# Kernel optimization log

Hardware: AMD Instinct MI355X
Metric: run time of the kernel (lower is better)

## Reference

```python
import jax, jax.numpy as jnp
import numpy as np

B, CIN, H, W = 8, 128, 64, 64
COUT = 128
UP = 2
KH = KW = 2 * UP  # 4
K = KH * KW       # 16
HO, WO = H - KH + 1, W - KW + 1  # stride=1, padding=0 (defaults actually used)


def setup_inputs() -> dict:
    key = jax.random.key(0)
    k1, k2, k3, k4, k5 = jax.random.split(key, 5)
    inp = jax.random.normal(k1, (B, CIN, H, W), jnp.float32)
    offset = jax.random.normal(k2, (B, 2 * K, HO, WO), jnp.float32)
    mask = jax.random.uniform(k3, (B, K, HO, WO), jnp.float32)
    fan_in = CIN * KH * KW
    bound = 1.0 / np.sqrt(fan_in)  # kaiming_uniform(a=sqrt(5)) bound
    weight = jax.random.uniform(k4, (COUT, CIN, KH, KW), jnp.float32, -bound, bound)
    bias = jax.random.uniform(k5, (COUT,), jnp.float32, -bound, bound)
    return {"input": inp, "offset": offset, "mask": mask, "weight": weight, "bias": bias}


def _deform_conv(inp, offset, mask, weight, bias):
    # modulated deformable conv, groups=1, stride=1, pad=0, dilation=1
    b, cin, h, w = inp.shape
    ho, wo = offset.shape[2], offset.shape[3]
    k = mask.shape[1]
    off = offset.reshape(b, k, 2, ho, wo)
    dy, dx = off[:, :, 0], off[:, :, 1]              # [b,k,ho,wo]

    ki, kj = jnp.meshgrid(jnp.arange(KH), jnp.arange(KW), indexing="ij")
    ki = ki.reshape(k).astype(inp.dtype)
    kj = kj.reshape(k).astype(inp.dtype)

    # sampling coords: base output pixel + kernel tap + learned offset
    y = dy + ki[None, :, None, None] + jnp.arange(ho, dtype=inp.dtype)[None, None, :, None]
    x = dx + kj[None, :, None, None] + jnp.arange(wo, dtype=inp.dtype)[None, None, None, :]

    y0f = jnp.floor(y)
    x0f = jnp.floor(x)
    wy = y - y0f                                     # [b,k,ho,wo]
    wx = x - x0f
    y0 = y0f.astype(jnp.int32)
    x0 = x0f.astype(jnp.int32)

    inp_flat = inp.reshape(b, cin, h * w)

    def gather(yy, xx):
        valid = (yy >= 0) & (yy < h) & (xx >= 0) & (xx < w)
        idx = (jnp.clip(yy, 0, h - 1) * w + jnp.clip(xx, 0, w - 1)).reshape(b, -1)
        v = jnp.take_along_axis(inp_flat, idx[:, None, :], axis=2)
        v = v.reshape(b, cin, k, ho, wo)
        return v * valid[:, None].astype(inp.dtype)

    v00 = gather(y0, x0)
    v01 = gather(y0, x0 + 1)
    v10 = gather(y0 + 1, x0)
    v11 = gather(y0 + 1, x0 + 1)

    wy = wy[:, None]  # [b,1,k,ho,wo]
    wx = wx[:, None]
    sampled = (v00 * (1 - wy) * (1 - wx) + v01 * (1 - wy) * wx
               + v10 * wy * (1 - wx) + v11 * wy * wx)
    sampled = sampled * mask[:, None]                # mask modulation

    # weight is flipped in forward: weight.flip(-1, -2)
    w_flip = weight[:, :, ::-1, ::-1].reshape(weight.shape[0], cin, k)
    out = jnp.einsum("bckhw,ock->bohw", sampled, w_flip)
    return out + bias[None, :, None, None]


def reference(input, offset, mask, weight, bias):
    return _deform_conv(input, offset, mask, weight, bias)
```

## Files before the change

### kernel.cpp

```cpp
#include <hip/hip_runtime.h>
#include <hip/hip_bf16.h>

#define B_    8
#define CIN   128
#define H_    64
#define W_    64
#define COUT  128
#define K_    16
#define HO    61
#define WO    61
#define HW_   (HO * WO)

typedef short bf16x8 __attribute__((ext_vector_type(8)));
typedef short s16x4  __attribute__((ext_vector_type(4)));
typedef int   s32x4  __attribute__((ext_vector_type(4)));
typedef float f32x4  __attribute__((ext_vector_type(4)));
typedef float f32x2  __attribute__((ext_vector_type(2)));
typedef float f32x4u __attribute__((ext_vector_type(4), aligned(4)));

__global__ __launch_bounds__(256) void prep_all(const float* __restrict__ inp,
                                                const float* __restrict__ w,
                                                __hip_bfloat16* __restrict__ T,
                                                __hip_bfloat16* __restrict__ A2) {
    const int t = threadIdx.x;
    if (blockIdx.x < 512) {
        __shared__ float ld[64][129];
        const int b  = blockIdx.x >> 6;
        const int sb = (blockIdx.x & 63) << 6;
        const float* src = inp + ((size_t)b << 19);
        #pragma unroll
        for (int i = 0; i < 8; ++i) {
            int j  = i * 256 + t;
            int c  = j >> 4;
            int s4 = (j & 15) << 2;
            f32x4u v = *(const f32x4u*)(const void*)(src + ((size_t)c << 12) + sb + s4);
            #pragma unroll
            for (int q = 0; q < 4; ++q) ld[s4 + q][c] = v[q];
        }
        __syncthreads();
        __hip_bfloat16* dst = T + (((size_t)b << 12) + sb) * 128;
        #pragma unroll
        for (int i = 0; i < 8; ++i) {
            int j  = i * 256 + t;
            int s  = j >> 5;
            int c4 = (j & 31) << 2;
            s16x4 v;
            #pragma unroll
            for (int q = 0; q < 4; ++q) {
                __hip_bfloat16 hh = __float2bfloat16(ld[s][c4 + q]);
                v[q] = *reinterpret_cast<const short*>(&hh);
            }
            *(s16x4*)(void*)(dst + (size_t)s * 128 + c4) = v;
        }
    } else {
        int gid  = (blockIdx.x - 512) * 256 + t;
        int lane = gid & 63;
        int it   = (gid >> 6) & 63;
        int blk  = gid >> 12;
        int o    = blk * 16 + (lane & 15);
        int kk   = it * 32 + (lane >> 4) * 8;
        int k    = kk >> 7;
        int c0   = kk & 127;
        const float* srcw = w + (((size_t)(o << 7) + c0) << 4) + (15 - k);
        __hip_bfloat16* dst = A2 + (size_t)gid * 8;
        #pragma unroll
        for (int j = 0; j < 8; ++j)
            dst[j] = __float2bfloat16(srcw[j << 4]);
    }
}

__global__ __launch_bounds__(512, 4) void deform_gather(
        const __hip_bfloat16* __restrict__ T, const float* __restrict__ off,
        const float* __restrict__ msk, const __hip_bfloat16* __restrict__ A2,
        const float* __restrict__ bias, float* __restrict__ out) {

    __shared__ __align__(16) __hip_bfloat16 Bs[2][64 * 128];
    __shared__ float pw[4][1024];
    __shared__ int   pb[2][1024];

    const int t   = threadIdx.x;
    const int bid = blockIdx.x;
    const int b   = bid & 7;
    const int ho  = bid >> 3;

    #pragma unroll
    for (int ii = 0; ii < 2; ++ii) {
        const int idx = ii * 512 + t;
        const int px  = idx & 63;
        const int k   = idx >> 6;
        const bool pvalid = (px < WO);
        const int wo_c = pvalid ? px : (WO - 1);
        const int r    = ho * WO + wo_c;
        const int ki = k >> 2, kj = k & 3;
        const size_t offb = (size_t)b * (2 * K_ * HW_);
        float dy = off[offb + (size_t)(2 * k)     * HW_ + r];
        float dx = off[offb + (size_t)(2 * k + 1) * HW_ + r];
        float mm = msk[(size_t)b * (K_ * HW_) + (size_t)k * HW_ + r];
        if (!pvalid) mm = 0.0f;

        float y   = dy + (float)(ki + ho);
        float x   = dx + (float)(kj + wo_c);
        float y0f = floorf(y), x0f = floorf(x);
        float wy  = y - y0f,   wx  = x - x0f;
        int y0 = (int)y0f, x0 = (int)x0f;
        int y1 = y0 + 1,   x1 = x0 + 1;

        float wy0v = (1.0f - wy) * ((y0 >= 0 && y0 < H_) ? mm : 0.0f);
        float wy1v = wy          * ((y1 >= 0 && y1 < H_) ? mm : 0.0f);
        int cy0 = min(max(y0, 0), H_ - 1), cy1 = min(max(y1, 0), H_ - 1);

        float wx0v = (1.0f - wx) * ((x0 >= 0 && x0 < W_) ? 1.0f : 0.0f);
        float wx1v = wx          * ((x1 >= 0 && x1 < W_) ? 1.0f : 0.0f);
        int xb = min(max(x0, 0), W_ - 2);
        int tsh = x0 - xb;
        float a0 = (tsh == 0) ? wx0v : ((tsh == -1) ? wx1v : 0.0f);
        float a1 = (tsh == 0) ? wx1v : ((tsh ==  1) ? wx0v : 0.0f);

        pw[0][idx] = wy0v * a0;  pw[1][idx] = wy0v * a1;
        pw[2][idx] = wy1v * a0;  pw[3][idx] = wy1v * a1;
        pb[0][idx] = (cy0 * W_ + xb) << 7;
        pb[1][idx] = (cy1 * W_ + xb) << 7;
    }
    __syncthreads();

    const int lane = t & 63;
    const int wv   = t >> 6;
    const int p_g  = lane >> 2;
    const int mrow = lane & 15;
    const int quad = lane >> 4;
    const __hip_bfloat16* Tb = T + ((size_t)b << 19);

    int rowU[2], cbU[2], swzU[2];
    #pragma unroll
    for (int i = 0; i < 2; ++i) {
        const int u = (wv << 1) + i;
        rowU[i] = ((u >> 2) << 4) + p_g;
        cbU[i]  = ((u & 3) << 5) + ((lane & 3) << 3);
        swzU[i] = (rowU[i] << 7) + (((cbU[i] >> 3) ^ (rowU[i] & 7)) << 3);
    }

    f32x4 accA = {0.f,0.f,0.f,0.f}, accB = {0.f,0.f,0.f,0.f};
    f32x4 accC = {0.f,0.f,0.f,0.f}, accD = {0.f,0.f,0.f,0.f};

    s32x4 cE[2][4], cO[2][4];
    bf16x8 avR[4];

    auto uget = [&](int qp, s32x4 (&cv)[2][4]) {
        #pragma unroll
        for (int i = 0; i < 2; ++i) {
            const int pidx = (qp << 6) + rowU[i];
            const __hip_bfloat16* p0 = Tb + pb[0][pidx] + cbU[i];
            const __hip_bfloat16* p1 = Tb + pb[1][pidx] + cbU[i];
            cv[i][0] = *(const s32x4*)(const void*)(p0);
            cv[i][1] = *(const s32x4*)(const void*)(p0 + 128);
            cv[i][2] = *(const s32x4*)(const void*)(p1);
            cv[i][3] = *(const s32x4*)(const void*)(p1 + 128);
        }
    };

    auto ucomb = [&](int qp, const s32x4 (&cv)[2][4]) {
        const int bb_ = qp & 1;
        #pragma unroll
        for (int i = 0; i < 2; ++i) {
            const int pidx = (qp << 6) + rowU[i];
            const float w0 = pw[0][pidx], w1 = pw[1][pidx];
            const float w2 = pw[2][pidx], w3 = pw[3][pidx];
            bf16x8 v;
            #pragma unroll
            for (int jj = 0; jj < 4; ++jj) {
                const unsigned a = (unsigned)cv[i][0][jj];
                const unsigned bq = (unsigned)cv[i][1][jj];
                const unsigned c = (unsigned)cv[i][2][jj];
                const unsigned d = (unsigned)cv[i][3][jj];
                f32x2 va = { __uint_as_float(a << 16),  __uint_as_float(a & 0xffff0000u) };
                f32x2 vb = { __uint_as_float(bq << 16), __uint_as_float(bq & 0xffff0000u) };
                f32x2 vc = { __uint_as_float(c << 16),  __uint_as_float(c & 0xffff0000u) };
                f32x2 vd = { __uint_as_float(d << 16),  __uint_as_float(d & 0xffff0000u) };
                f32x2 s = va * w0;
                s += vb * w1;
                s += vc * w2;
                s += vd * w3;
                __hip_bfloat16 h0 = __float2bfloat16(s[0]);
                __hip_bfloat16 h1 = __float2bfloat16(s[1]);
                v[2*jj]   = *reinterpret_cast<const short*>(&h0);
                v[2*jj+1] = *reinterpret_cast<const short*>(&h1);
            }
            *(bf16x8*)(void*)(&Bs[bb_][swzU[i]]) = v;
        }
    };

    auto loadA = [&](int qp) {
        #pragma unroll
        for (int s_ = 0; s_ < 4; ++s_) {
            avR[s_] = *(const bf16x8*)(const void*)(
                A2 + ((size_t)((wv * 64 + qp * 4 + s_) * 64 + lane) << 3));
        }
    };

    auto mfma_exec = [&](int qp) {
        const int bb_ = qp & 1;
        const int mx = mrow & 7;
        #pragma unroll
        for (int s_ = 0; s_ < 4; ++s_) {
            const int colX = ((((s_ << 2) + quad) ^ mx) << 3);
            const int i0 = (mrow << 7) + colX;
            const int i1 = ((16 + mrow) << 7) + colX;
            const int i2 = ((32 + mrow) << 7) + colX;
            const int i3 = ((48 + mrow) << 7) + colX;
            bf16x8 b0 = *(const bf16x8*)(const void*)(&Bs[bb_][i0]);
            bf16x8 b1 = *(const bf16x8*)(const void*)(&Bs[bb_][i1]);
            bf16x8 b2 = *(const bf16x8*)(const void*)(&Bs[bb_][i2]);
            bf16x8 b3 = *(const bf16x8*)(const void*)(&Bs[bb_][i3]);
            accA = __builtin_amdgcn_mfma_f32_16x16x32_bf16(avR[s_], b0, accA, 0, 0, 0);
            accB = __builtin_amdgcn_mfma_f32_16x16x32_bf16(avR[s_], b1, accB, 0, 0, 0);
            accC = __builtin_amdgcn_mfma_f32_16x16x32_bf16(avR[s_], b2, accC, 0, 0, 0);
            accD = __builtin_amdgcn_mfma_f32_16x16x32_bf16(avR[s_], b3, accD, 0, 0, 0);
        }
    };

    uget(0, cE);
    uget(1, cO);
    loadA(0);
    ucomb(0, cE);
    __syncthreads();

    #pragma unroll 1
    for (int qq = 1; qq < 15; qq += 2) {
        uget(qq + 1, cE);
        __builtin_amdgcn_s_setprio(1);
        mfma_exec(qq - 1);
        __builtin_amdgcn_s_setprio(0);
        loadA(qq);
        ucomb(qq, cO);
        __syncthreads();
        uget(qq + 2, cO);
        __builtin_amdgcn_s_setprio(1);
        mfma_exec(qq);
        __builtin_amdgcn_s_setprio(0);
        loadA(qq + 1);
        ucomb(qq + 1, cE);
        __syncthreads();
    }
    __builtin_amdgcn_s_setprio(1);
    mfma_exec(14);
    __builtin_amdgcn_s_setprio(0);
    loadA(15);
    ucomb(15, cO);
    __syncthreads();
    mfma_exec(15);

    #pragma unroll
    for (int pg = 0; pg < 4; ++pg) {
        const int px = (pg << 4) + mrow;
        if (px < WO) {
            const size_t outb = (size_t)b * (COUT * HW_) + (size_t)(ho * WO + px);
            const f32x4 a = (pg == 0) ? accA : (pg == 1) ? accB
                          : (pg == 2) ? accC : accD;
            #pragma unroll
            for (int jj = 0; jj < 4; ++jj) {
                const int o = wv * 16 + quad * 4 + jj;
                out[outb + (size_t)o * HW_] = a[jj] + bias[o];
            }
        }
    }
}

extern "C" void kernel_launch(void* const* d_in, const int* in_sizes, int n_in,
                              void* d_out, int out_size, void* d_ws, size_t ws_size,
                              hipStream_t stream) {
    const float* inp  = (const float*)d_in[0];
    const float* off  = (const float*)d_in[1];
    const float* msk  = (const float*)d_in[2];
    const float* wgt  = (const float*)d_in[3];
    const float* bias = (const float*)d_in[4];
    float* out = (float*)d_out;

    __hip_bfloat16* A2 = (__hip_bfloat16*)d_ws;
    __hip_bfloat16* T  = (__hip_bfloat16*)((char*)d_ws + (1 << 20));

    prep_all<<<640, 256, 0, stream>>>(inp, wgt, T, A2);

    int nblk = B_ * HO;
    deform_gather<<<nblk, 512, 0, stream>>>(T, off, msk, A2, bias, out);
}
```

Measured before the change: 117.5 us.

## Drop two-deep gather prefetch to single buffer and use raw LDS barrier

```diff
diff --git a/kernel.cpp b/kernel.cpp
--- a/kernel.cpp
+++ b/kernel.cpp
@@ -17,6 +17,8 @@
 typedef float f32x4  __attribute__((ext_vector_type(4)));
 typedef float f32x2  __attribute__((ext_vector_type(2)));
 typedef float f32x4u __attribute__((ext_vector_type(4), aligned(4)));
+
+#define RAWBAR() asm volatile("s_waitcnt lgkmcnt(0)\n\ts_barrier" ::: "memory")
 
 __global__ __launch_bounds__(256) void prep_all(const float* __restrict__ inp,
                                                 const float* __restrict__ w,
@@ -142,23 +144,23 @@
     f32x4 accA = {0.f,0.f,0.f,0.f}, accB = {0.f,0.f,0.f,0.f};
     f32x4 accC = {0.f,0.f,0.f,0.f}, accD = {0.f,0.f,0.f,0.f};
 
-    s32x4 cE[2][4], cO[2][4];
+    s32x4 cU[2][4];
     bf16x8 avR[4];
 
-    auto uget = [&](int qp, s32x4 (&cv)[2][4]) {
+    auto uget = [&](int qp) {
         #pragma unroll
         for (int i = 0; i < 2; ++i) {
             const int pidx = (qp << 6) + rowU[i];
             const __hip_bfloat16* p0 = Tb + pb[0][pidx] + cbU[i];
             const __hip_bfloat16* p1 = Tb + pb[1][pidx] + cbU[i];
-            cv[i][0] = *(const s32x4*)(const void*)(p0);
-            cv[i][1] = *(const s32x4*)(const void*)(p0 + 128);
-            cv[i][2] = *(const s32x4*)(const void*)(p1);
-            cv[i][3] = *(const s32x4*)(const void*)(p1 + 128);
-        }
-    };
-
-    auto ucomb = [&](int qp, const s32x4 (&cv)[2][4]) {
+            cU[i][0] = *(const s32x4*)(const void*)(p0);
+            cU[i][1] = *(const s32x4*)(const void*)(p0 + 128);
+            cU[i][2] = *(const s32x4*)(const void*)(p1);
+            cU[i][3] = *(const s32x4*)(const void*)(p1 + 128);
+        }
+    };
+
+    auto ucomb = [&](int qp) {
         const int bb_ = qp & 1;
         #pragma unroll
         for (int i = 0; i < 2; ++i) {
@@ -168,10 +170,10 @@
             bf16x8 v;
             #pragma unroll
             for (int jj = 0; jj < 4; ++jj) {
-                const unsigned a = (unsigned)cv[i][0][jj];
-                const unsigned bq = (unsigned)cv[i][1][jj];
-                const unsigned c = (unsigned)cv[i][2][jj];
-                const unsigned d = (unsigned)cv[i][3][jj];
+                const unsigned a = (unsigned)cU[i][0][jj];
+                const unsigned bq = (unsigned)cU[i][1][jj];
+                const unsigned c = (unsigned)cU[i][2][jj];
+                const unsigned d = (unsigned)cU[i][3][jj];
                 f32x2 va = { __uint_as_float(a << 16),  __uint_as_float(a & 0xffff0000u) };
                 f32x2 vb = { __uint_as_float(bq << 16), __uint_as_float(bq & 0xffff0000u) };
                 f32x2 vc = { __uint_as_float(c << 16),  __uint_as_float(c & 0xffff0000u) };
@@ -218,35 +220,21 @@
         }
     };
 
-    uget(0, cE);
-    uget(1, cO);
+    uget(0);
+    ucomb(0);
     loadA(0);
-    ucomb(0, cE);
-    __syncthreads();
+    RAWBAR();
 
     #pragma unroll 1
-    for (int qq = 1; qq < 15; qq += 2) {
-        uget(qq + 1, cE);
+    for (int qp = 1; qp < 16; ++qp) {
+        uget(qp);
         __builtin_amdgcn_s_setprio(1);
-        mfma_exec(qq - 1);
+        mfma_exec(qp - 1);
         __builtin_amdgcn_s_setprio(0);
-        loadA(qq);
-        ucomb(qq, cO);
-        __syncthreads();
-        uget(qq + 2, cO);
-        __builtin_amdgcn_s_setprio(1);
-        mfma_exec(qq);
-        __builtin_amdgcn_s_setprio(0);
-        loadA(qq + 1);
-        ucomb(qq + 1, cE);
-        __syncthreads();
-    }
-    __builtin_amdgcn_s_setprio(1);
-    mfma_exec(14);
-    __builtin_amdgcn_s_setprio(0);
-    loadA(15);
-    ucomb(15, cO);
-    __syncthreads();
+        loadA(qp);
+        ucomb(qp);
+        RAWBAR();
+    }
     mfma_exec(15);
 
     #pragma unroll
```

After: 113.7 us. 1.03x faster.
